# Performance work log

Measured on AMD Instinct MI355X. Metric: run time of the kernel, lower is better.

The kernel has to match this reference:

```python
import jax, jax.numpy as jnp
import numpy as np
import math

D_MODEL = 1024
H = 16
D_K = D_MODEL // H          # 64
D_HALF = D_MODEL // 2       # 512
DH = D_HALF // H            # 32 (half head dim for q/k)
B, S = 2, 1024
LAMBDA_INIT = 0.8 - 0.6 * math.exp(-0.3 * (1 - 1))  # layer_index=1 -> 0.2


def setup_inputs() -> dict:
    key = jax.random.key(0)
    ks = jax.random.split(key, 20)
    def lin(kk, fan_in, fan_out):
        lim = 1.0 / math.sqrt(fan_in)
        kw, kb = jax.random.split(kk)
        W = jax.random.uniform(kw, (fan_in, fan_out), jnp.float32, -lim, lim)
        b = jax.random.uniform(kb, (fan_out,), jnp.float32, -lim, lim)
        return W, b
    Wq1, bq1 = lin(ks[0], D_MODEL, D_HALF)
    Wq2, bq2 = lin(ks[1], D_MODEL, D_HALF)
    Wk1, bk1 = lin(ks[2], D_MODEL, D_HALF)
    Wk2, bk2 = lin(ks[3], D_MODEL, D_HALF)
    Wv, bv = lin(ks[4], D_MODEL, D_MODEL)
    Wo, bo = lin(ks[5], D_MODEL, D_MODEL)
    q = jax.random.normal(ks[6], (B, S, D_MODEL), jnp.float32)
    k = jax.random.normal(ks[7], (B, S, D_MODEL), jnp.float32)
    v = jax.random.normal(ks[8], (B, S, D_MODEL), jnp.float32)
    # causal 0/1 mask, already 4-D [B,1,S,S]
    mask = jnp.broadcast_to(jnp.tril(jnp.ones((S, S), jnp.int32)), (B, 1, S, S))
    # small random lambda scalars (torch inits to 0 -> degenerate gradients)
    lq1 = jax.random.normal(ks[9], (1,), jnp.float32) * 0.1
    lk1 = jax.random.normal(ks[10], (1,), jnp.float32) * 0.1
    lq2 = jax.random.normal(ks[11], (1,), jnp.float32) * 0.1
    lk2 = jax.random.normal(ks[12], (1,), jnp.float32) * 0.1
    return dict(q=q, k=k, v=v, mask=mask,
                Wq1=Wq1, bq1=bq1, Wq2=Wq2, bq2=bq2,
                Wk1=Wk1, bk1=bk1, Wk2=Wk2, bk2=bk2,
                Wv=Wv, bv=bv, Wo=Wo, bo=bo,
                lq1=lq1, lk1=lk1, lq2=lq2, lk2=lk2)


def reference(q, k, v, mask, Wq1, bq1, Wq2, bq2, Wk1, bk1, Wk2, bk2,
              Wv, bv, Wo, bo, lq1, lk1, lq2, lk2):
    b, sq, _ = q.shape
    sk = k.shape[1]
    # projections, reshaped to [B, S, H, head_dim]
    q1 = (q @ Wq1 + bq1).reshape(b, sq, H, DH)
    q2 = (q @ Wq2 + bq2).reshape(b, sq, H, DH)
    k1 = (k @ Wk1 + bk1).reshape(b, sk, H, DH)
    k2 = (k @ Wk2 + bk2).reshape(b, sk, H, DH)
    vv = (v @ Wv + bv).reshape(b, sk, H, D_K)
    lam = jnp.exp(lq1 * lk1) - jnp.exp(lq2 * lk2) + LAMBDA_INIT  # shape (1,)
    scale = 1.0 / math.sqrt(D_K)
    s1 = jnp.einsum('bqhd,bkhd->bhqk', q1, k1) * scale
    s2 = jnp.einsum('bqhd,bkhd->bhqk', q2, k2) * scale
    neg = jnp.float32(-1e9)
    keep = mask != 0  # [B,1,Sq,Sk], broadcasts over heads
    s1 = jnp.where(keep, s1, neg)
    s2 = jnp.where(keep, s2, neg)
    a1 = jax.nn.softmax(s1, axis=-1)
    a2 = jax.nn.softmax(s2, axis=-1)
    diff = a1 - lam[0] * a2  # dropout p=0.0 -> identity
    out = jnp.einsum('bhqk,bkhd->bqhd', diff, vv).reshape(b, sq, D_MODEL)
    return out @ Wo + bo
```

## Files before the change

kernel.cpp:

```cpp
#include <hip/hip_runtime.h>
#include <hip/hip_bf16.h>
#include <cstdint>
#include <cstddef>

typedef __attribute__((ext_vector_type(8))) short short8;
typedef __attribute__((ext_vector_type(4))) float floatx4;

#define B_ 2
#define S_ 1024
#define H_ 16
#define DM_ 1024
#define DHALF_ 512
#define DH_ 32
#define DK_ 64
#define LAMBDA_INIT_ 0.2f
#define SCALE_ 0.125f
#define M_INIT_ -1.0e4f
#define MASK_NEG_ -1.0e9f

static __device__ __forceinline__ unsigned short f2bf(float f) {
  uint32_t u = __float_as_uint(f);
  uint32_t r = (u + 0x7fffu + ((u >> 16) & 1u)) >> 16;
  return (unsigned short)r;
}

static __device__ __forceinline__ uint32_t pkbf(float a, float b) {
  __hip_bfloat162 h = __float22bfloat162_rn(make_float2(a, b));
  return *reinterpret_cast<uint32_t*>(&h);
}

static __device__ __forceinline__ void gload16(const void* g, void* l) {
  __builtin_amdgcn_global_load_lds(
      (const __attribute__((address_space(1))) uint32_t*)g,
      (__attribute__((address_space(3))) uint32_t*)l, 16, 0, 0);
}

__global__ __launch_bounds__(256) void prep_kernel(
    const float* __restrict__ q, const float* __restrict__ k, const float* __restrict__ v,
    const float* __restrict__ Wq1, const float* __restrict__ Wq2,
    const float* __restrict__ Wk1, const float* __restrict__ Wk2,
    const float* __restrict__ Wv, const float* __restrict__ Wo,
    const float* __restrict__ bq1, const float* __restrict__ bq2,
    const float* __restrict__ bk1, const float* __restrict__ bk2,
    unsigned short* __restrict__ WqT, unsigned short* __restrict__ WkT,
    unsigned short* __restrict__ WvT, unsigned short* __restrict__ WoT,
    unsigned short* __restrict__ qbf, unsigned short* __restrict__ kbf,
    unsigned short* __restrict__ vbf,
    float* __restrict__ biasQ, float* __restrict__ biasK)
{
  __shared__ float tile[64][65];
  const int bid = blockIdx.x;
  const int tid = threadIdx.x;
  if (bid < 1024) {
    const float* W; unsigned short* WT; int ncols, n_off, local;
    if (bid < 128)      { W = Wq1; WT = WqT; ncols = 512;  n_off = 0;   local = bid; }
    else if (bid < 256) { W = Wq2; WT = WqT; ncols = 512;  n_off = 512; local = bid - 128; }
    else if (bid < 384) { W = Wk1; WT = WkT; ncols = 512;  n_off = 0;   local = bid - 256; }
    else if (bid < 512) { W = Wk2; WT = WkT; ncols = 512;  n_off = 512; local = bid - 384; }
    else if (bid < 768) { W = Wv;  WT = WvT; ncols = 1024; n_off = 0;   local = bid - 512; }
    else                { W = Wo;  WT = WoT; ncols = 1024; n_off = 0;   local = bid - 768; }
    const int ntiles = ncols >> 6;
    const int n0 = (local % ntiles) * 64;
    const int k0 = (local / ntiles) * 64;
#pragma unroll
    for (int i = 0; i < 4; ++i) {
      int idx = tid + 256 * i;
      int r = idx >> 4, c4 = idx & 15;
      float4 val = *reinterpret_cast<const float4*>(W + (size_t)(k0 + r) * ncols + n0 + c4 * 4);
      tile[r][c4 * 4 + 0] = val.x; tile[r][c4 * 4 + 1] = val.y;
      tile[r][c4 * 4 + 2] = val.z; tile[r][c4 * 4 + 3] = val.w;
    }
    __syncthreads();
#pragma unroll
    for (int i = 0; i < 2; ++i) {
      int G = tid + 256 * i;
      int n = G >> 3, g = G & 7;
      short8 o;
#pragma unroll
      for (int j = 0; j < 8; ++j) o[j] = (short)f2bf(tile[g * 8 + j][n]);
      *reinterpret_cast<short8*>(WT + (size_t)(n_off + n0 + n) * 1024 + k0 + g * 8) = o;
    }
  } else if (bid < 4096) {
    int local = bid - 1024;
    int t = local >> 10;
    int i = local & 1023;
    const float* src = (t == 0) ? q : ((t == 1) ? k : v);
    unsigned short* dst = (t == 0) ? qbf : ((t == 1) ? kbf : vbf);
    const int base = i * 2048 + tid * 8;
    float4 a = *reinterpret_cast<const float4*>(src + base);
    float4 b2 = *reinterpret_cast<const float4*>(src + base + 4);
    short8 o;
    o[0] = (short)f2bf(a.x);  o[1] = (short)f2bf(a.y);
    o[2] = (short)f2bf(a.z);  o[3] = (short)f2bf(a.w);
    o[4] = (short)f2bf(b2.x); o[5] = (short)f2bf(b2.y);
    o[6] = (short)f2bf(b2.z); o[7] = (short)f2bf(b2.w);
    *reinterpret_cast<short8*>(dst + base) = o;
  } else {
#pragma unroll
    for (int j = 0; j < 4; ++j) {
      int i = j * 256 + tid;
      biasQ[i] = (i < 512) ? bq1[i] : bq2[i - 512];
      biasK[i] = (i < 512) ? bk1[i] : bk2[i - 512];
    }
  }
}

#define STAGE(Gbase, row0, kk0, L)                                            \
  {                                                                           \
    _Pragma("unroll")                                                         \
    for (int i_ = 0; i_ < 4; ++i_) {                                          \
      const int o_ = i_ * 4096 + tid * 16;           \
      const int r_ = o_ >> 7;                       \
      const int c_ = ((o_ >> 4) & 7) ^ (r_ & 7);                              \
      gload16(Gbase + (size_t)(row0 + r_) * 1024 + (kk0) + c_ * 8,            \
              (L) + (o_ >> 1));                                               \
    }                                                                         \
  }

static __device__ __forceinline__ void gemm_mainloop(
    const unsigned short* __restrict__ A, const unsigned short* __restrict__ BT,
    int m0, int n0,
    unsigned short* As0, unsigned short* As1,
    unsigned short* Bs0, unsigned short* Bs1,
    floatx4 (&acc)[4][4])
{
  const int tid = threadIdx.x;
  const int lane = tid & 63;
  const int l15 = lane & 15, hi = lane >> 4;
  const int wid = tid >> 6;
  const int wr = wid >> 1, wc = wid & 1;

  STAGE(A, m0, 0, As0);
  STAGE(BT, n0, 0, Bs0);
  __syncthreads();

  for (int ks = 0; ks < 16; ++ks) {
    unsigned short* Ac = (ks & 1) ? As1 : As0;
    unsigned short* Bc = (ks & 1) ? Bs1 : Bs0;
    unsigned short* An = (ks & 1) ? As0 : As1;
    unsigned short* Bn = (ks & 1) ? Bs0 : Bs1;
    if (ks < 15) {
      STAGE(A, m0, (ks + 1) * 64, An);
      STAGE(BT, n0, (ks + 1) * 64, Bn);
    }
#pragma unroll
    for (int kk = 0; kk < 2; ++kk) {
      short8 af[4], bf[4];
#pragma unroll
      for (int mt = 0; mt < 4; ++mt) {
        const int r = wr * 64 + mt * 16 + l15;
        af[mt] = *reinterpret_cast<const short8*>(Ac + r * 64 + (((kk * 4 + hi) ^ (r & 7)) << 3));
      }
#pragma unroll
      for (int nt = 0; nt < 4; ++nt) {
        const int r = wc * 64 + nt * 16 + l15;
        bf[nt] = *reinterpret_cast<const short8*>(Bc + r * 64 + (((kk * 4 + hi) ^ (r & 7)) << 3));
      }
#pragma unroll
      for (int mt = 0; mt < 4; ++mt)
#pragma unroll
        for (int nt = 0; nt < 4; ++nt)
          acc[mt][nt] = __builtin_amdgcn_mfma_f32_16x16x32_bf16(af[mt], bf[nt], acc[mt][nt], 0, 0, 0);
    }
    __syncthreads();
  }
}

__global__ __launch_bounds__(256) void proj_gemm_kernel(
    const unsigned short* __restrict__ qbf, const unsigned short* __restrict__ kbf,
    const unsigned short* __restrict__ vbf,
    const unsigned short* __restrict__ WqT, const unsigned short* __restrict__ WkT,
    const unsigned short* __restrict__ WvT,
    const float* __restrict__ biasQ, const float* __restrict__ biasK,
    const float* __restrict__ bv,
    unsigned short* __restrict__ q12b, unsigned short* __restrict__ k12b,
    unsigned short* __restrict__ vvT)
{
  __shared__ unsigned short As[2][128 * 64];
  __shared__ unsigned short Bs[2][128 * 64];
  const int z = blockIdx.z;
  const unsigned short* A = (z == 0) ? qbf : ((z == 1) ? kbf : vbf);
  const unsigned short* BT = (z == 0) ? WqT : ((z == 1) ? WkT : WvT);
  const float* bias = (z == 0) ? biasQ : ((z == 1) ? biasK : bv);
  const int n0 = blockIdx.x * 128;
  const int m0 = blockIdx.y * 128;
  const int lane = threadIdx.x & 63, wid = threadIdx.x >> 6;
  const int l15 = lane & 15, hi = lane >> 4;
  const int wr = wid >> 1, wc = wid & 1;

  floatx4 acc[4][4];
#pragma unroll
  for (int a = 0; a < 4; ++a)
#pragma unroll
    for (int c = 0; c < 4; ++c) acc[a][c] = (floatx4){0.f, 0.f, 0.f, 0.f};

  gemm_mainloop(A, BT, m0, n0, As[0], As[1], Bs[0], Bs[1], acc);

#pragma unroll
  for (int nt = 0; nt < 4; ++nt) {
    const int n = n0 + wc * 64 + nt * 16 + l15;
    const float bn = bias[n];
#pragma unroll
    for (int mt = 0; mt < 4; ++mt) {
      const int mrow = m0 + wr * 64 + mt * 16 + 4 * hi;
      if (z < 2) {
        unsigned short* dst = (z == 0 ? q12b : k12b);
#pragma unroll
        for (int r = 0; r < 4; ++r)
          dst[(size_t)(mrow + r) * 1024 + n] = f2bf(acc[mt][nt][r] + bn);
      } else {
        const int bb = mrow >> 10, ss = mrow & 1023;
        const int hh = n >> 6, dd = n & 63;
        float v0 = acc[mt][nt][0] + bn, v1 = acc[mt][nt][1] + bn;
        float v2 = acc[mt][nt][2] + bn, v3 = acc[mt][nt][3] + bn;
        uint2 pk;
        pk.x = pkbf(v0, v1);
        pk.y = pkbf(v2, v3);
        *reinterpret_cast<uint2*>(vvT + ((size_t)(bb * 16 + hh) * 64 + dd) * 1024 + ss) = pk;
      }
    }
  }
}

__global__ __launch_bounds__(256) void out_gemm_kernel(
    const unsigned short* __restrict__ Ab, const unsigned short* __restrict__ BT,
    const float* __restrict__ bias, float* __restrict__ out)
{
  __shared__ unsigned short As[2][128 * 64];
  __shared__ unsigned short Bs[2][128 * 64];
  const int n0 = blockIdx.x * 128;
  const int m0 = blockIdx.y * 128;
  const int lane = threadIdx.x & 63, wid = threadIdx.x >> 6;
  const int l15 = lane & 15, hi = lane >> 4;
  const int wr = wid >> 1, wc = wid & 1;

  floatx4 acc[4][4];
#pragma unroll
  for (int a = 0; a < 4; ++a)
#pragma unroll
    for (int c = 0; c < 4; ++c) acc[a][c] = (floatx4){0.f, 0.f, 0.f, 0.f};

  gemm_mainloop(Ab, BT, m0, n0, As[0], As[1], Bs[0], Bs[1], acc);

#pragma unroll
  for (int nt = 0; nt < 4; ++nt) {
    const int n = n0 + wc * 64 + nt * 16 + l15;
    const float bn = bias[n];
#pragma unroll
    for (int mt = 0; mt < 4; ++mt) {
      const int mrow = m0 + wr * 64 + mt * 16 + 4 * hi;
#pragma unroll
      for (int r = 0; r < 4; ++r)
        out[(size_t)(mrow + r) * 1024 + n] = acc[mt][nt][r] + bn;
    }
  }
}

#define STAGE_KV(kbase_, bi_)                                                  \
  {                                                                            \
    const size_t krow0_ = (size_t)(b * S_ + (kbase_));                         \
    _Pragma("unroll")                                                          \
    for (int i_ = 0; i_ < 2; ++i_) {                                           \
      const int o_ = i_ * 4096 + tid * 16;               \
      const int r_ = o_ >> 7;                           \
      const int c_ = ((o_ >> 4) & 7) ^ (r_ & 7);                               \
      const unsigned short* ks_ = (c_ < 4)                                     \
          ? (k12b + (krow0_ + r_) * DM_ + h * DH_ + c_ * 8)                    \
          : (k12b + (krow0_ + r_) * DM_ + DHALF_ + h * DH_ + (c_ - 4) * 8);    \
      gload16(ks_, &Kt[bi_][0] + (o_ >> 1));                                   \
      const unsigned short* vs_ = vvT + (vrow0 + r_) * (size_t)S_ +            \
                                  (kbase_) + c_ * 8;                           \
      gload16(vs_, &Vt[bi_][0] + (o_ >> 1));                                   \
    }                                                                          \
  }

__global__ __launch_bounds__(256) void diff_attn_kernel(
    const unsigned short* __restrict__ q12b, const unsigned short* __restrict__ k12b,
    const unsigned short* __restrict__ vvT, unsigned short* __restrict__ attn,
    const float* __restrict__ lq1, const float* __restrict__ lk1,
    const float* __restrict__ lq2, const float* __restrict__ lk2)
{
  __shared__ unsigned short Kt[2][64 * 64];
  __shared__ unsigned short Vt[2][64 * 64];
  __shared__ unsigned short Pl[4][2][16 * 64];

  const int tid = threadIdx.x;
  const int lane = tid & 63, wid = tid >> 6;
  const int l15 = lane & 15, hi = lane >> 4;

  const int idx = blockIdx.x;
  const int hf = idx >> 8;
  const int pk = idx & 255;
  const int h = pk & 15;
  const int b = (pk >> 4) & 1;
  const int j = pk >> 5;
  const int qblk = hf ? (15 - j) : j;

  const int qbase = qblk * 64 + wid * 16;
  const float lam = __expf(lq1[0] * lk1[0]) - __expf(lq2[0] * lk2[0]) + LAMBDA_INIT_;
  const size_t vrow0 = (size_t)(b * H_ + h) * DK_;

  const size_t qrow = (size_t)(b * S_ + qbase + l15) * DM_;
  const short8 q1f = *reinterpret_cast<const short8*>(q12b + qrow + h * DH_ + hi * 8);
  const short8 q2f = *reinterpret_cast<const short8*>(q12b + qrow + DHALF_ + h * DH_ + hi * 8);

  floatx4 acc1[4], acc2[4];
#pragma unroll
  for (int dt = 0; dt < 4; ++dt) {
    acc1[dt] = (floatx4){0.f, 0.f, 0.f, 0.f};
    acc2[dt] = (floatx4){0.f, 0.f, 0.f, 0.f};
  }
  float m1 = M_INIT_, m2 = M_INIT_, l1 = 0.f, l2 = 0.f;

  unsigned short* P1 = &Pl[wid][0][0];
  unsigned short* P2 = &Pl[wid][1][0];

  const int ntiles = qblk + 1;
  STAGE_KV(0, 0);
  __syncthreads();

  for (int kb = 0; kb < ntiles; ++kb) {
    const int cur = kb & 1;
    const int kbase = kb * 64;
    if (kb + 1 < ntiles) STAGE_KV(kbase + 64, cur ^ 1);

    floatx4 s1[4], s2[4];
    const floatx4 zz = (floatx4){0.f, 0.f, 0.f, 0.f};
#pragma unroll
    for (int t = 0; t < 4; ++t) {
      const int r = 16 * t + l15;
      short8 k1f = *reinterpret_cast<const short8*>(&Kt[cur][0] + r * 64 + ((hi ^ (r & 7)) << 3));
      short8 k2f = *reinterpret_cast<const short8*>(&Kt[cur][0] + r * 64 + (((hi + 4) ^ (r & 7)) << 3));
      s1[t] = __builtin_amdgcn_mfma_f32_16x16x32_bf16(k1f, q1f, zz, 0, 0, 0);
      s2[t] = __builtin_amdgcn_mfma_f32_16x16x32_bf16(k2f, q2f, zz, 0, 0, 0);
    }

    if (kb == ntiles - 1) {
      const int qg = qbase + l15;
#pragma unroll
      for (int t = 0; t < 4; ++t) {
#pragma unroll
        for (int r = 0; r < 4; ++r) {
          const int kg = kbase + 16 * t + 4 * hi + r;
          if (kg > qg) { s1[t][r] = MASK_NEG_; s2[t][r] = MASK_NEG_; }
        }
      }
    }

    float tm1, tm2;
    {
      float a1 = fmaxf(fmaxf(s1[0][0], s1[0][1]), fmaxf(s1[0][2], s1[0][3]));
      float b1 = fmaxf(fmaxf(s1[1][0], s1[1][1]), fmaxf(s1[1][2], s1[1][3]));
      float c1 = fmaxf(fmaxf(s1[2][0], s1[2][1]), fmaxf(s1[2][2], s1[2][3]));
      float d1 = fmaxf(fmaxf(s1[3][0], s1[3][1]), fmaxf(s1[3][2], s1[3][3]));
      tm1 = fmaxf(fmaxf(a1, b1), fmaxf(c1, d1));
      float a2 = fmaxf(fmaxf(s2[0][0], s2[0][1]), fmaxf(s2[0][2], s2[0][3]));
      float b2 = fmaxf(fmaxf(s2[1][0], s2[1][1]), fmaxf(s2[1][2], s2[1][3]));
      float c2 = fmaxf(fmaxf(s2[2][0], s2[2][1]), fmaxf(s2[2][2], s2[2][3]));
      float d2 = fmaxf(fmaxf(s2[3][0], s2[3][1]), fmaxf(s2[3][2], s2[3][3]));
      tm2 = fmaxf(fmaxf(a2, b2), fmaxf(c2, d2));
    }
    tm1 = fmaxf(tm1, __shfl_xor(tm1, 16));
    tm1 = fmaxf(tm1, __shfl_xor(tm1, 32));
    tm2 = fmaxf(tm2, __shfl_xor(tm2, 16));
    tm2 = fmaxf(tm2, __shfl_xor(tm2, 32));

    const float nm1 = fmaxf(m1, tm1);
    const float nm2 = fmaxf(m2, tm2);
    const float sc1 = __expf((m1 - nm1) * SCALE_);
    const float sc2 = __expf((m2 - nm2) * SCALE_);
    m1 = nm1; m2 = nm2;

    float rs1 = 0.f, rs2 = 0.f;
#pragma unroll
    for (int t = 0; t < 4; ++t) {
      float p10 = __expf((s1[t][0] - m1) * SCALE_);
      float p11 = __expf((s1[t][1] - m1) * SCALE_);
      float p12 = __expf((s1[t][2] - m1) * SCALE_);
      float p13 = __expf((s1[t][3] - m1) * SCALE_);
      rs1 += (p10 + p11) + (p12 + p13);
      float p20 = __expf((s2[t][0] - m2) * SCALE_);
      float p21 = __expf((s2[t][1] - m2) * SCALE_);
      float p22 = __expf((s2[t][2] - m2) * SCALE_);
      float p23 = __expf((s2[t][3] - m2) * SCALE_);
      rs2 += (p20 + p21) + (p22 + p23);
      const int idx2 = l15 * 64 + (((2 * t + (hi >> 1)) ^ (l15 & 7)) << 3) + ((hi & 1) << 2);
      uint2 w1; w1.x = pkbf(p10, p11); w1.y = pkbf(p12, p13);
      *reinterpret_cast<uint2*>(P1 + idx2) = w1;
      uint2 w2; w2.x = pkbf(p20, p21); w2.y = pkbf(p22, p23);
      *reinterpret_cast<uint2*>(P2 + idx2) = w2;
    }
    rs1 += __shfl_xor(rs1, 16);
    rs1 += __shfl_xor(rs1, 32);
    rs2 += __shfl_xor(rs2, 16);
    rs2 += __shfl_xor(rs2, 32);
    l1 = l1 * sc1 + rs1;
    l2 = l2 * sc2 + rs2;

#pragma unroll
    for (int dt = 0; dt < 4; ++dt) { acc1[dt] *= sc1; acc2[dt] *= sc2; }

#pragma unroll
    for (int kc = 0; kc < 2; ++kc) {
      const int q = l15;
      short8 p1f = *reinterpret_cast<const short8*>(P1 + q * 64 + (((hi + 4 * kc) ^ (q & 7)) << 3));
      short8 p2f = *reinterpret_cast<const short8*>(P2 + q * 64 + (((hi + 4 * kc) ^ (q & 7)) << 3));
#pragma unroll
      for (int dt = 0; dt < 4; ++dt) {
        const int d = dt * 16 + l15;
        short8 vf = *reinterpret_cast<const short8*>(&Vt[cur][0] + d * 64 + (((hi + 4 * kc) ^ (d & 7)) << 3));
        acc1[dt] = __builtin_amdgcn_mfma_f32_16x16x32_bf16(vf, p1f, acc1[dt], 0, 0, 0);
        acc2[dt] = __builtin_amdgcn_mfma_f32_16x16x32_bf16(vf, p2f, acc2[dt], 0, 0, 0);
      }
    }
    __syncthreads();
  }

  const float inv1 = 1.0f / l1;
  const float inv2 = lam / l2;
  const int qg = qbase + l15;
  unsigned short* op = attn + (size_t)(b * S_ + qg) * DM_ + h * DK_;
#pragma unroll
  for (int dt = 0; dt < 4; ++dt) {
    float o0 = acc1[dt][0] * inv1 - acc2[dt][0] * inv2;
    float o1 = acc1[dt][1] * inv1 - acc2[dt][1] * inv2;
    float o2 = acc1[dt][2] * inv1 - acc2[dt][2] * inv2;
    float o3 = acc1[dt][3] * inv1 - acc2[dt][3] * inv2;
    uint2 pkv;
    pkv.x = pkbf(o0, o1);
    pkv.y = pkbf(o2, o3);
    *reinterpret_cast<uint2*>(op + dt * 16 + 4 * hi) = pkv;
  }
}

extern "C" void kernel_launch(void* const* d_in, const int* in_sizes, int n_in,
                              void* d_out, int out_size, void* d_ws, size_t ws_size,
                              hipStream_t stream)
{
  const float* q   = (const float*)d_in[0];
  const float* k   = (const float*)d_in[1];
  const float* v   = (const float*)d_in[2];
  const float* Wq1 = (const float*)d_in[4];
  const float* bq1 = (const float*)d_in[5];
  const float* Wq2 = (const float*)d_in[6];
  const float* bq2 = (const float*)d_in[7];
  const float* Wk1 = (const float*)d_in[8];
  const float* bk1 = (const float*)d_in[9];
  const float* Wk2 = (const float*)d_in[10];
  const float* bk2 = (const float*)d_in[11];
  const float* Wv  = (const float*)d_in[12];
  const float* bv  = (const float*)d_in[13];
  const float* Wo  = (const float*)d_in[14];
  const float* bo  = (const float*)d_in[15];
  const float* lq1 = (const float*)d_in[16];
  const float* lk1 = (const float*)d_in[17];
  const float* lq2 = (const float*)d_in[18];
  const float* lk2 = (const float*)d_in[19];
  float* out = (float*)d_out;

  uint8_t* w = (uint8_t*)d_ws;
  unsigned short* WqT  = (unsigned short*)w; w += (size_t)2 * 1024 * 1024;
  unsigned short* WkT  = (unsigned short*)w; w += (size_t)2 * 1024 * 1024;
  unsigned short* WvT  = (unsigned short*)w; w += (size_t)2 * 1024 * 1024;
  unsigned short* WoT  = (unsigned short*)w; w += (size_t)2 * 1024 * 1024;
  unsigned short* qbf  = (unsigned short*)w; w += (size_t)4 * 1024 * 1024;
  unsigned short* kbf  = (unsigned short*)w; w += (size_t)4 * 1024 * 1024;
  unsigned short* vbf  = (unsigned short*)w; w += (size_t)4 * 1024 * 1024;
  unsigned short* q12b = (unsigned short*)w; w += (size_t)4 * 1024 * 1024;
  unsigned short* k12b = (unsigned short*)w; w += (size_t)4 * 1024 * 1024;
  unsigned short* vvT  = (unsigned short*)w; w += (size_t)4 * 1024 * 1024;
  float* biasQ = (float*)w; w += 4096;
  float* biasK = (float*)w; w += 4096;
  unsigned short* attnb = qbf;

  dim3 blk(256);
  hipLaunchKernelGGL(prep_kernel, dim3(4097), blk, 0, stream,
                     q, k, v, Wq1, Wq2, Wk1, Wk2, Wv, Wo,
                     bq1, bq2, bk1, bk2,
                     WqT, WkT, WvT, WoT, qbf, kbf, vbf, biasQ, biasK);

  hipLaunchKernelGGL(proj_gemm_kernel, dim3(8, 16, 3), blk, 0, stream,
                     qbf, kbf, vbf, WqT, WkT, WvT, biasQ, biasK, bv,
                     q12b, k12b, vvT);

  hipLaunchKernelGGL(diff_attn_kernel, dim3(512), blk, 0, stream,
                     q12b, k12b, vvT, attnb, lq1, lk1, lq2, lk2);

  hipLaunchKernelGGL(out_gemm_kernel, dim3(8, 16), blk, 0, stream,
                     attnb, WoT, bo, out);
}
```

Baseline: 83.95 us.

## Shrink GEMM tiles for more blocks and widen attention KV tiles to 128

The GEMM mainloop is templated on tile size. The projection GEMM now uses 128x64 tiles and the output GEMM 64x64 tiles, which multiplies the block count so more of the device's compute units get work. The attention kernel now stages 128-key K/V tiles, halving the number of barrier-separated iterations. It also splits softmax and the PV MFMAs into two 64-key halves so exp work and matrix ops interleave, with s_setprio raising priority around the MFMA sections. The cost is more LDS per attention block and smaller per-block reuse in the GEMMs.

```diff
diff --git a/kernel.cpp b/kernel.cpp
--- a/kernel.cpp
+++ b/kernel.cpp
@@ -105,33 +105,37 @@
   }
 }
 
-#define STAGE(Gbase, row0, kk0, L)                                            \
-  {                                                                           \
-    _Pragma("unroll")                                                         \
-    for (int i_ = 0; i_ < 4; ++i_) {                                          \
-      const int o_ = i_ * 4096 + tid * 16;           \
-      const int r_ = o_ >> 7;                       \
-      const int c_ = ((o_ >> 4) & 7) ^ (r_ & 7);                              \
-      gload16(Gbase + (size_t)(row0 + r_) * 1024 + (kk0) + c_ * 8,            \
-              (L) + (o_ >> 1));                                               \
-    }                                                                         \
-  }
-
+template<int ROWS>
+static __device__ __forceinline__ void stage_rows(
+    const unsigned short* __restrict__ G, int row0, int kk0,
+    unsigned short* L, int tid)
+{
+#pragma unroll
+  for (int i = 0; i < ROWS / 32; ++i) {
+    const int o = i * 4096 + tid * 16;
+    const int r = o >> 7;
+    const int c = ((o >> 4) & 7) ^ (r & 7);
+    gload16(G + (size_t)(row0 + r) * 1024 + kk0 + c * 8, L + (o >> 1));
+  }
+}
+
+template<int BM, int BN>
 static __device__ __forceinline__ void gemm_mainloop(
     const unsigned short* __restrict__ A, const unsigned short* __restrict__ BT,
     int m0, int n0,
     unsigned short* As0, unsigned short* As1,
     unsigned short* Bs0, unsigned short* Bs1,
-    floatx4 (&acc)[4][4])
-{
+    floatx4 (&acc)[BM / 32][BN / 32])
+{
+  constexpr int MT = BM / 32, NT = BN / 32;
   const int tid = threadIdx.x;
   const int lane = tid & 63;
   const int l15 = lane & 15, hi = lane >> 4;
   const int wid = tid >> 6;
   const int wr = wid >> 1, wc = wid & 1;
 
-  STAGE(A, m0, 0, As0);
-  STAGE(BT, n0, 0, Bs0);
+  stage_rows<BM>(A, m0, 0, As0, tid);
+  stage_rows<BN>(BT, n0, 0, Bs0, tid);
   __syncthreads();
 
   for (int ks = 0; ks < 16; ++ks) {
@@ -140,26 +144,26 @@
     unsigned short* An = (ks & 1) ? As0 : As1;
     unsigned short* Bn = (ks & 1) ? Bs0 : Bs1;
     if (ks < 15) {
-      STAGE(A, m0, (ks + 1) * 64, An);
-      STAGE(BT, n0, (ks + 1) * 64, Bn);
+      stage_rows<BM>(A, m0, (ks + 1) * 64, An, tid);
+      stage_rows<BN>(BT, n0, (ks + 1) * 64, Bn, tid);
     }
 #pragma unroll
     for (int kk = 0; kk < 2; ++kk) {
-      short8 af[4], bf[4];
-#pragma unroll
-      for (int mt = 0; mt < 4; ++mt) {
-        const int r = wr * 64 + mt * 16 + l15;
+      short8 af[MT], bf[NT];
+#pragma unroll
+      for (int mt = 0; mt < MT; ++mt) {
+        const int r = wr * (BM / 2) + mt * 16 + l15;
         af[mt] = *reinterpret_cast<const short8*>(Ac + r * 64 + (((kk * 4 + hi) ^ (r & 7)) << 3));
       }
 #pragma unroll
-      for (int nt = 0; nt < 4; ++nt) {
-        const int r = wc * 64 + nt * 16 + l15;
+      for (int nt = 0; nt < NT; ++nt) {
+        const int r = wc * (BN / 2) + nt * 16 + l15;
         bf[nt] = *reinterpret_cast<const short8*>(Bc + r * 64 + (((kk * 4 + hi) ^ (r & 7)) << 3));
       }
 #pragma unroll
-      for (int mt = 0; mt < 4; ++mt)
-#pragma unroll
-        for (int nt = 0; nt < 4; ++nt)
+      for (int mt = 0; mt < MT; ++mt)
+#pragma unroll
+        for (int nt = 0; nt < NT; ++nt)
           acc[mt][nt] = __builtin_amdgcn_mfma_f32_16x16x32_bf16(af[mt], bf[nt], acc[mt][nt], 0, 0, 0);
     }
     __syncthreads();
@@ -177,28 +181,28 @@
     unsigned short* __restrict__ vvT)
 {
   __shared__ unsigned short As[2][128 * 64];
-  __shared__ unsigned short Bs[2][128 * 64];
+  __shared__ unsigned short Bs[2][64 * 64];
   const int z = blockIdx.z;
   const unsigned short* A = (z == 0) ? qbf : ((z == 1) ? kbf : vbf);
   const unsigned short* BT = (z == 0) ? WqT : ((z == 1) ? WkT : WvT);
   const float* bias = (z == 0) ? biasQ : ((z == 1) ? biasK : bv);
-  const int n0 = blockIdx.x * 128;
+  const int n0 = blockIdx.x * 64;
   const int m0 = blockIdx.y * 128;
   const int lane = threadIdx.x & 63, wid = threadIdx.x >> 6;
   const int l15 = lane & 15, hi = lane >> 4;
   const int wr = wid >> 1, wc = wid & 1;
 
-  floatx4 acc[4][4];
+  floatx4 acc[4][2];
 #pragma unroll
   for (int a = 0; a < 4; ++a)
 #pragma unroll
-    for (int c = 0; c < 4; ++c) acc[a][c] = (floatx4){0.f, 0.f, 0.f, 0.f};
-
-  gemm_mainloop(A, BT, m0, n0, As[0], As[1], Bs[0], Bs[1], acc);
-
-#pragma unroll
-  for (int nt = 0; nt < 4; ++nt) {
-    const int n = n0 + wc * 64 + nt * 16 + l15;
+    for (int c = 0; c < 2; ++c) acc[a][c] = (floatx4){0.f, 0.f, 0.f, 0.f};
+
+  gemm_mainloop<128, 64>(A, BT, m0, n0, As[0], As[1], Bs[0], Bs[1], acc);
+
+#pragma unroll
+  for (int nt = 0; nt < 2; ++nt) {
+    const int n = n0 + wc * 32 + nt * 16 + l15;
     const float bn = bias[n];
 #pragma unroll
     for (int mt = 0; mt < 4; ++mt) {
@@ -226,29 +230,29 @@
     const unsigned short* __restrict__ Ab, const unsigned short* __restrict__ BT,
     const float* __restrict__ bias, float* __restrict__ out)
 {
-  __shared__ unsigned short As[2][128 * 64];
-  __shared__ unsigned short Bs[2][128 * 64];
-  const int n0 = blockIdx.x * 128;
-  const int m0 = blockIdx.y * 128;
+  __shared__ unsigned short As[2][64 * 64];
+  __shared__ unsigned short Bs[2][64 * 64];
+  const int n0 = blockIdx.x * 64;
+  const int m0 = blockIdx.y * 64;
   const int lane = threadIdx.x & 63, wid = threadIdx.x >> 6;
   const int l15 = lane & 15, hi = lane >> 4;
   const int wr = wid >> 1, wc = wid & 1;
 
-  floatx4 acc[4][4];
-#pragma unroll
-  for (int a = 0; a < 4; ++a)
-#pragma unroll
-    for (int c = 0; c < 4; ++c) acc[a][c] = (floatx4){0.f, 0.f, 0.f, 0.f};
-
-  gemm_mainloop(Ab, BT, m0, n0, As[0], As[1], Bs[0], Bs[1], acc);
-
-#pragma unroll
-  for (int nt = 0; nt < 4; ++nt) {
-    const int n = n0 + wc * 64 + nt * 16 + l15;
+  floatx4 acc[2][2];
+#pragma unroll
+  for (int a = 0; a < 2; ++a)
+#pragma unroll
+    for (int c = 0; c < 2; ++c) acc[a][c] = (floatx4){0.f, 0.f, 0.f, 0.f};
+
+  gemm_mainloop<64, 64>(Ab, BT, m0, n0, As[0], As[1], Bs[0], Bs[1], acc);
+
+#pragma unroll
+  for (int nt = 0; nt < 2; ++nt) {
+    const int n = n0 + wc * 32 + nt * 16 + l15;
     const float bn = bias[n];
 #pragma unroll
-    for (int mt = 0; mt < 4; ++mt) {
-      const int mrow = m0 + wr * 64 + mt * 16 + 4 * hi;
+    for (int mt = 0; mt < 2; ++mt) {
+      const int mrow = m0 + wr * 32 + mt * 16 + 4 * hi;
 #pragma unroll
       for (int r = 0; r < 4; ++r)
         out[(size_t)(mrow + r) * 1024 + n] = acc[mt][nt][r] + bn;
@@ -260,17 +264,18 @@
   {                                                                            \
     const size_t krow0_ = (size_t)(b * S_ + (kbase_));                         \
     _Pragma("unroll")                                                          \
-    for (int i_ = 0; i_ < 2; ++i_) {                                           \
-      const int o_ = i_ * 4096 + tid * 16;               \
-      const int r_ = o_ >> 7;                           \
-      const int c_ = ((o_ >> 4) & 7) ^ (r_ & 7);                               \
-      const unsigned short* ks_ = (c_ < 4)                                     \
-          ? (k12b + (krow0_ + r_) * DM_ + h * DH_ + c_ * 8)                    \
-          : (k12b + (krow0_ + r_) * DM_ + DHALF_ + h * DH_ + (c_ - 4) * 8);    \
+    for (int i_ = 0; i_ < 4; ++i_) {                                           \
+      const int o_ = i_ * 4096 + tid * 16;              \
+      const int kr_ = o_ >> 7;                         \
+      const int kc_ = ((o_ >> 4) & 7) ^ (kr_ & 7);                             \
+      const unsigned short* ks_ = (kc_ < 4)                                    \
+          ? (k12b + (krow0_ + kr_) * DM_ + h * DH_ + kc_ * 8)                  \
+          : (k12b + (krow0_ + kr_) * DM_ + DHALF_ + h * DH_ + (kc_ - 4) * 8);  \
       gload16(ks_, &Kt[bi_][0] + (o_ >> 1));                                   \
-      const unsigned short* vs_ = vvT + (vrow0 + r_) * (size_t)S_ +            \
-                                  (kbase_) + c_ * 8;                           \
-      gload16(vs_, &Vt[bi_][0] + (o_ >> 1));                                   \
+      const int vr_ = o_ >> 8;                          \
+      const int vc_ = ((o_ >> 4) & 15) ^ (vr_ & 15);                           \
+      gload16(vvT + (vrow0 + vr_) * (size_t)S_ + (kbase_) + vc_ * 8,           \
+              &Vt[bi_][0] + (o_ >> 1));                                        \
     }                                                                          \
   }
 
@@ -280,8 +285,8 @@
     const float* __restrict__ lq1, const float* __restrict__ lk1,
     const float* __restrict__ lq2, const float* __restrict__ lk2)
 {
-  __shared__ unsigned short Kt[2][64 * 64];
-  __shared__ unsigned short Vt[2][64 * 64];
+  __shared__ unsigned short Kt[2][128 * 64];
+  __shared__ unsigned short Vt[2][64 * 128];
   __shared__ unsigned short Pl[4][2][16 * 64];
 
   const int tid = threadIdx.x;
@@ -315,50 +320,50 @@
   unsigned short* P1 = &Pl[wid][0][0];
   unsigned short* P2 = &Pl[wid][1][0];
 
-  const int ntiles = qblk + 1;
+  const int ntiles = (qblk >> 1) + 1;
   STAGE_KV(0, 0);
   __syncthreads();
 
   for (int kb = 0; kb < ntiles; ++kb) {
     const int cur = kb & 1;
-    const int kbase = kb * 64;
-    if (kb + 1 < ntiles) STAGE_KV(kbase + 64, cur ^ 1);
-
-    floatx4 s1[4], s2[4];
+    const int kbase = kb * 128;
+    if (kb + 1 < ntiles) STAGE_KV(kbase + 128, cur ^ 1);
+
+    floatx4 s1[8], s2[8];
     const floatx4 zz = (floatx4){0.f, 0.f, 0.f, 0.f};
-#pragma unroll
-    for (int t = 0; t < 4; ++t) {
+    __builtin_amdgcn_s_setprio(1);
+#pragma unroll
+    for (int t = 0; t < 8; ++t) {
       const int r = 16 * t + l15;
       short8 k1f = *reinterpret_cast<const short8*>(&Kt[cur][0] + r * 64 + ((hi ^ (r & 7)) << 3));
       short8 k2f = *reinterpret_cast<const short8*>(&Kt[cur][0] + r * 64 + (((hi + 4) ^ (r & 7)) << 3));
       s1[t] = __builtin_amdgcn_mfma_f32_16x16x32_bf16(k1f, q1f, zz, 0, 0, 0);
       s2[t] = __builtin_amdgcn_mfma_f32_16x16x32_bf16(k2f, q2f, zz, 0, 0, 0);
     }
+    __builtin_amdgcn_s_setprio(0);
 
     if (kb == ntiles - 1) {
       const int qg = qbase + l15;
 #pragma unroll
-      for (int t = 0; t < 4; ++t) {
-#pragma unroll
-        for (int r = 0; r < 4; ++r) {
-          const int kg = kbase + 16 * t + 4 * hi + r;
-          if (kg > qg) { s1[t][r] = MASK_NEG_; s2[t][r] = MASK_NEG_; }
+      for (int t = 0; t < 8; ++t) {
+#pragma unroll
+        for (int e = 0; e < 4; ++e) {
+          const int kg = kbase + 16 * t + 4 * hi + e;
+          if (kg > qg) { s1[t][e] = MASK_NEG_; s2[t][e] = MASK_NEG_; }
         }
       }
     }
 
     float tm1, tm2;
     {
-      float a1 = fmaxf(fmaxf(s1[0][0], s1[0][1]), fmaxf(s1[0][2], s1[0][3]));
-      float b1 = fmaxf(fmaxf(s1[1][0], s1[1][1]), fmaxf(s1[1][2], s1[1][3]));
-      float c1 = fmaxf(fmaxf(s1[2][0], s1[2][1]), fmaxf(s1[2][2], s1[2][3]));
-      float d1 = fmaxf(fmaxf(s1[3][0], s1[3][1]), fmaxf(s1[3][2], s1[3][3]));
-      tm1 = fmaxf(fmaxf(a1, b1), fmaxf(c1, d1));
-      float a2 = fmaxf(fmaxf(s2[0][0], s2[0][1]), fmaxf(s2[0][2], s2[0][3]));
-      float b2 = fmaxf(fmaxf(s2[1][0], s2[1][1]), fmaxf(s2[1][2], s2[1][3]));
-      float c2 = fmaxf(fmaxf(s2[2][0], s2[2][1]), fmaxf(s2[2][2], s2[2][3]));
-      float d2 = fmaxf(fmaxf(s2[3][0], s2[3][1]), fmaxf(s2[3][2], s2[3][3]));
-      tm2 = fmaxf(fmaxf(a2, b2), fmaxf(c2, d2));
+      float x1 = fmaxf(fmaxf(s1[0][0], s1[0][1]), fmaxf(s1[0][2], s1[0][3]));
+      float x2 = fmaxf(fmaxf(s2[0][0], s2[0][1]), fmaxf(s2[0][2], s2[0][3]));
+#pragma unroll
+      for (int t = 1; t < 8; ++t) {
+        x1 = fmaxf(x1, fmaxf(fmaxf(s1[t][0], s1[t][1]), fmaxf(s1[t][2], s1[t][3])));
+        x2 = fmaxf(x2, fmaxf(fmaxf(s2[t][0], s2[t][1]), fmaxf(s2[t][2], s2[t][3])));
+      }
+      tm1 = x1; tm2 = x2;
     }
     tm1 = fmaxf(tm1, __shfl_xor(tm1, 16));
     tm1 = fmaxf(tm1, __shfl_xor(tm1, 32));
@@ -370,25 +375,46 @@
     const float sc1 = __expf((m1 - nm1) * SCALE_);
     const float sc2 = __expf((m2 - nm2) * SCALE_);
     m1 = nm1; m2 = nm2;
+#pragma unroll
+    for (int dt = 0; dt < 4; ++dt) { acc1[dt] *= sc1; acc2[dt] *= sc2; }
 
     float rs1 = 0.f, rs2 = 0.f;
 #pragma unroll
-    for (int t = 0; t < 4; ++t) {
-      float p10 = __expf((s1[t][0] - m1) * SCALE_);
-      float p11 = __expf((s1[t][1] - m1) * SCALE_);
-      float p12 = __expf((s1[t][2] - m1) * SCALE_);
-      float p13 = __expf((s1[t][3] - m1) * SCALE_);
-      rs1 += (p10 + p11) + (p12 + p13);
-      float p20 = __expf((s2[t][0] - m2) * SCALE_);
-      float p21 = __expf((s2[t][1] - m2) * SCALE_);
-      float p22 = __expf((s2[t][2] - m2) * SCALE_);
-      float p23 = __expf((s2[t][3] - m2) * SCALE_);
-      rs2 += (p20 + p21) + (p22 + p23);
-      const int idx2 = l15 * 64 + (((2 * t + (hi >> 1)) ^ (l15 & 7)) << 3) + ((hi & 1) << 2);
-      uint2 w1; w1.x = pkbf(p10, p11); w1.y = pkbf(p12, p13);
-      *reinterpret_cast<uint2*>(P1 + idx2) = w1;
-      uint2 w2; w2.x = pkbf(p20, p21); w2.y = pkbf(p22, p23);
-      *reinterpret_cast<uint2*>(P2 + idx2) = w2;
+    for (int half = 0; half < 2; ++half) {
+#pragma unroll
+      for (int tt = 0; tt < 4; ++tt) {
+        const int t = half * 4 + tt;
+        float p10 = __expf((s1[t][0] - m1) * SCALE_);
+        float p11 = __expf((s1[t][1] - m1) * SCALE_);
+        float p12 = __expf((s1[t][2] - m1) * SCALE_);
+        float p13 = __expf((s1[t][3] - m1) * SCALE_);
+        rs1 += (p10 + p11) + (p12 + p13);
+        float p20 = __expf((s2[t][0] - m2) * SCALE_);
+        float p21 = __expf((s2[t][1] - m2) * SCALE_);
+        float p22 = __expf((s2[t][2] - m2) * SCALE_);
+        float p23 = __expf((s2[t][3] - m2) * SCALE_);
+        rs2 += (p20 + p21) + (p22 + p23);
+        const int idx2 = l15 * 64 + (((2 * tt + (hi >> 1)) ^ (l15 & 7)) << 3) + ((hi & 1) << 2);
+        uint2 w1; w1.x = pkbf(p10, p11); w1.y = pkbf(p12, p13);
+        *reinterpret_cast<uint2*>(P1 + idx2) = w1;
+        uint2 w2; w2.x = pkbf(p20, p21); w2.y = pkbf(p22, p23);
+        *reinterpret_cast<uint2*>(P2 + idx2) = w2;
+      }
+      __builtin_amdgcn_s_setprio(1);
+#pragma unroll
+      for (int kc = 0; kc < 2; ++kc) {
+        short8 p1f = *reinterpret_cast<const short8*>(P1 + l15 * 64 + (((hi + 4 * kc) ^ (l15 & 7)) << 3));
+        short8 p2f = *reinterpret_cast<const short8*>(P2 + l15 * 64 + (((hi + 4 * kc) ^ (l15 & 7)) << 3));
+#pragma unroll
+        for (int dt = 0; dt < 4; ++dt) {
+          const int d = dt * 16 + l15;
+          short8 vf = *reinterpret_cast<const short8*>(
+              &Vt[cur][0] + d * 128 + (((hi + 4 * (2 * half + kc)) ^ (d & 15)) << 3));
+          acc1[dt] = __builtin_amdgcn_mfma_f32_16x16x32_bf16(vf, p1f, acc1[dt], 0, 0, 0);
+          acc2[dt] = __builtin_amdgcn_mfma_f32_16x16x32_bf16(vf, p2f, acc2[dt], 0, 0, 0);
+        }
+      }
+      __builtin_amdgcn_s_setprio(0);
     }
     rs1 += __shfl_xor(rs1, 16);
     rs1 += __shfl_xor(rs1, 32);
@@ -397,22 +423,6 @@
     l1 = l1 * sc1 + rs1;
     l2 = l2 * sc2 + rs2;
 
-#pragma unroll
-    for (int dt = 0; dt < 4; ++dt) { acc1[dt] *= sc1; acc2[dt] *= sc2; }
-
-#pragma unroll
-    for (int kc = 0; kc < 2; ++kc) {
-      const int q = l15;
-      short8 p1f = *reinterpret_cast<const short8*>(P1 + q * 64 + (((hi + 4 * kc) ^ (q & 7)) << 3));
-      short8 p2f = *reinterpret_cast<const short8*>(P2 + q * 64 + (((hi + 4 * kc) ^ (q & 7)) << 3));
-#pragma unroll
-      for (int dt = 0; dt < 4; ++dt) {
-        const int d = dt * 16 + l15;
-        short8 vf = *reinterpret_cast<const short8*>(&Vt[cur][0] + d * 64 + (((hi + 4 * kc) ^ (d & 7)) << 3));
-        acc1[dt] = __builtin_amdgcn_mfma_f32_16x16x32_bf16(vf, p1f, acc1[dt], 0, 0, 0);
-        acc2[dt] = __builtin_amdgcn_mfma_f32_16x16x32_bf16(vf, p2f, acc2[dt], 0, 0, 0);
-      }
-    }
     __syncthreads();
   }
 
@@ -479,13 +489,13 @@
                      bq1, bq2, bk1, bk2,
                      WqT, WkT, WvT, WoT, qbf, kbf, vbf, biasQ, biasK);
 
-  hipLaunchKernelGGL(proj_gemm_kernel, dim3(8, 16, 3), blk, 0, stream,
+  hipLaunchKernelGGL(proj_gemm_kernel, dim3(16, 16, 3), blk, 0, stream,
                      qbf, kbf, vbf, WqT, WkT, WvT, biasQ, biasK, bv,
                      q12b, k12b, vvT);
 
   hipLaunchKernelGGL(diff_attn_kernel, dim3(512), blk, 0, stream,
                      q12b, k12b, vvT, attnb, lq1, lk1, lq2, lk2);
 
-  hipLaunchKernelGGL(out_gemm_kernel, dim3(8, 16), blk, 0, stream,
+  hipLaunchKernelGGL(out_gemm_kernel, dim3(16, 32), blk, 0, stream,
                      attnb, WoT, bo, out);
 }
```

Result: faster. 78.27 us (-6.8%).
